# Optimization experiments

Measured on AMD Instinct MI355X. Metric: run time of the kernel, lower is better.

## Reference

```python
import jax, jax.numpy as jnp
import numpy as np

EPS = 1e-5  # BatchNorm2d default eps


def setup_inputs() -> dict:
    key = jax.random.key(0)
    k1, k2, k3, k4 = jax.random.split(key, 4)
    B, C, S, E = 2, 512, 256, 512  # C == E is required by the module's math
    x = jax.random.normal(k1, (B, C, S, E), dtype=jnp.float32)
    Q = jax.random.normal(k2, (E, E), dtype=jnp.float32)
    K = jax.random.normal(k3, (E, E), dtype=jnp.float32)
    V = jax.random.normal(k4, (E, E), dtype=jnp.float32)
    return {"x": x, "Q": Q, "K": K, "V": V}


def reference(x, Q, K, V):
    # BatchNorm2d(affine=False), training-mode batch stats over (B, H, W)
    mean = jnp.mean(x, axis=(0, 2, 3), keepdims=True)
    var = jnp.var(x, axis=(0, 2, 3), keepdims=True)  # biased, matches torch normalization
    xn = (x - mean) * jax.lax.rsqrt(var + EPS)

    divisor = jnp.sqrt(jnp.asarray(x.shape[-1], dtype=x.dtype))
    q = jnp.einsum('bcse,ef->bcsf', xn, Q)
    k = jnp.einsum('bcse,ef->bcsf', xn, K)
    v = jnp.einsum('bcse,ef->bcsf', xn, V)

    # scores: [B, C, S, S]
    prod = jnp.einsum('bcsf,bctf->bcst', q, k) / divisor
    # nn.Softmax2d softmaxes over the CHANNEL dim (axis 1)
    sm = jax.nn.softmax(prod, axis=1)
    attention = jnp.einsum('bcst,bctf->bcsf', sm, v)
    # dropout is identity in eval/reference mode; residual since E_in == E_out
    return attention + xn
```

## Files before the change

### kernel.cpp

```cpp
#include <hip/hip_runtime.h>
#include <hip/hip_bf16.h>
#include <cstdio>

#define Bn 2
#define Cn 512
#define Sn 256
#define En 512

typedef __attribute__((ext_vector_type(8))) short bf16x8;
typedef __attribute__((ext_vector_type(4))) float f32x4;

static constexpr size_t PROD_B = (1ull << 20);
static constexpr size_t V_B    = PROD_B + (256ull << 20);
static constexpr size_t ATH_B  = V_B + (256ull << 20);
static constexpr size_t ATL_B  = ATH_B + (512ull << 10);
static constexpr size_t VT_B   = ATL_B + (512ull << 10);
static constexpr size_t XNH_B  = VT_B + (512ull << 10);
static constexpr size_t XNL_B  = XNH_B + (256ull << 20);
static constexpr size_t WS_BIG = XNL_B + (256ull << 20);
static constexpr size_t SMT_B  = XNL_B;

__device__ __forceinline__ unsigned short f2bf(float f) {
  union { __hip_bfloat16 h; unsigned short u; } cv;
  cv.h = __float2bfloat16(f);
  return cv.u;
}
__device__ __forceinline__ float bf2f(unsigned short u) {
  union { unsigned int i; float f; } cv;
  cv.i = ((unsigned int)u) << 16;
  return cv.f;
}
__device__ __forceinline__ void split2(float v, unsigned short& h, unsigned short& l) {
  h = f2bf(v);
  l = f2bf(v - bf2f(h));
}
__device__ __forceinline__ int swzc(int row, int col) {
  return row * 64 + ((col & 3) | ((col & 60) ^ ((row & 7) << 3)));
}
__device__ __forceinline__ bf16x8 ldfrag(const unsigned short* arr, int row, int ks, int lane) {
  const int byte = (ks * 64 + ((lane >> 4) << 4)) ^ ((row & 7) << 4);
  return *(const bf16x8*)((const char*)(arr + (size_t)row * 64) + byte);
}
__device__ __forceinline__ f32x4 MFMA(bf16x8 a, bf16x8 b, f32x4 c) {
  return __builtin_amdgcn_mfma_f32_16x16x32_bf16(a, b, c, 0, 0, 0);
}
__device__ __forceinline__ void glds16(const void* g, void* l) {
  __builtin_amdgcn_global_load_lds(
      (const __attribute__((address_space(1))) unsigned int*)g,
      (__attribute__((address_space(3))) unsigned int*)l, 16, 0, 0);
}
__device__ __forceinline__ void stage_tile(const unsigned short* g, unsigned short* l,
                                           int nbytes, int wid, int lane, int nwaves) {
  const char* gb = (const char*)g;
  char* lb = (char*)l;
  for (int j = wid; j < (nbytes >> 10); j += nwaves)
    glds16(gb + j * 1024 + lane * 16, lb + j * 1024);
}

__global__ void k1_stats(const float* __restrict__ x, float* __restrict__ ws) {
  const int c = blockIdx.x, tid = threadIdx.x;
  const float4* p0 = (const float4*)(x + (size_t)c * (Sn * En));
  const float4* p1 = (const float4*)(x + (size_t)(Cn + c) * (Sn * En));
  float s1 = 0.f, s2 = 0.f;
  for (int i = tid; i < (Sn * En / 4); i += 256) {
    float4 a = p0[i], b = p1[i];
    s1 += (a.x + a.y) + (a.z + a.w) + (b.x + b.y) + (b.z + b.w);
    s2 += (a.x * a.x + a.y * a.y) + (a.z * a.z + a.w * a.w) +
          (b.x * b.x + b.y * b.y) + (b.z * b.z + b.w * b.w);
  }
  __shared__ float r1[256], r2[256];
  r1[tid] = s1; r2[tid] = s2;
  __syncthreads();
  for (int off = 128; off > 0; off >>= 1) {
    if (tid < off) { r1[tid] += r1[tid + off]; r2[tid] += r2[tid + off]; }
    __syncthreads();
  }
  if (tid == 0) {
    const float n = (float)(2 * Sn * En);
    float mean = r1[0] / n;
    float var = r2[0] / n - mean * mean;
    ws[c] = mean;
    ws[512 + c] = 1.0f / sqrtf(var + 1e-5f);
  }
}

__global__ void kA(const float* __restrict__ Q, const float* __restrict__ K,
                   const float* __restrict__ V, unsigned short* __restrict__ ATh,
                   unsigned short* __restrict__ ATl, unsigned short* __restrict__ VT) {
  const int f = blockIdx.x, tid = threadIdx.x;
  __shared__ float Kf[512];
  for (int i = tid; i < 512; i += 256) Kf[i] = K[(size_t)f * 512 + i];
  __syncthreads();
  const int fr64 = f & 63;
  const size_t atbase = ((size_t)(f >> 6) * 8) * 4096 + (size_t)fr64 * 64;
  const size_t vtbase = ((size_t)(f >> 7) * 8) * 8192 + (size_t)(f & 127) * 64;
#pragma unroll
  for (int half = 0; half < 2; ++half) {
    const int e = tid + half * 256;
    const float* Qe = Q + (size_t)e * 512;
    float acc = 0.f;
    for (int t = 0; t < 512; t += 4) {
      float4 q = *(const float4*)(Qe + t);
      acc += q.x * Kf[t] + q.y * Kf[t + 1] + q.z * Kf[t + 2] + q.w * Kf[t + 3];
    }
    unsigned short h, l;
    split2(acc, h, l);
    const int et = e >> 6, ec = e & 63;
    const int swa = (ec & 3) | ((ec & 60) ^ ((fr64 & 7) << 3));
    ATh[atbase + (size_t)et * 4096 + swa] = h;
    ATl[atbase + (size_t)et * 4096 + swa] = l;
    const int swv = (ec & 3) | ((ec & 60) ^ ((f & 7) << 3));
    VT[vtbase + (size_t)et * 8192 + swv] = f2bf(V[(size_t)e * 512 + f]);
  }
}

__global__ void kxn(const float* __restrict__ x, const float* __restrict__ ws,
                    unsigned short* __restrict__ XNh, unsigned short* __restrict__ XNl) {
  const int bid = blockIdx.x;
  const int bc = bid >> 1, half = bid & 1;
  const int c = bc & 511;
  const float mean = ws[c], rstd = ws[512 + c];
  const float* xb = x + (size_t)bc * 131072 + (size_t)half * 128 * 512;
  const int tid = threadIdx.x;
#pragma unroll 4
  for (int i = 0; i < 64; ++i) {
    const int g = tid + i * 256;
    const int r = g >> 7, c4 = g & 127;
    const float4 xv = *(const float4*)(xb + (size_t)r * 512 + c4 * 4);
    ushort4 hv, lv;
    split2((xv.x - mean) * rstd, hv.x, lv.x);
    split2((xv.y - mean) * rstd, hv.y, lv.y);
    split2((xv.z - mean) * rstd, hv.z, lv.z);
    split2((xv.w - mean) * rstd, hv.w, lv.w);
    const int et = c4 >> 4, colt4 = c4 & 15;
    const int row = half * 128 + r;
    const size_t idx = ((size_t)(bc * 8 + et) * 256 + row) * 64 +
                       ((colt4 * 4) ^ ((row & 7) << 3));
    *(ushort4*)&XNh[idx] = hv;
    *(ushort4*)&XNl[idx] = lv;
  }
}

__launch_bounds__(256)
__global__ void kv_proj(const unsigned short* __restrict__ VT,
                        const unsigned short* __restrict__ XNh_g,
                        unsigned short* __restrict__ vT_out) {
  __shared__ unsigned short BUF[2][16384];
  const int bid = blockIdx.x;
  const int L = (bid & 7) * 1024 + (bid >> 3);
  const int bc = L >> 3;
  const int fq = (L >> 1) & 3;
  const int th = L & 1;
  const int f0 = fq * 128, t0 = th * 128;
  const int tid = threadIdx.x, w = tid >> 6, lane = tid & 63;

  f32x4 acc[2][8];
#pragma unroll
  for (int i = 0; i < 2; ++i)
#pragma unroll
    for (int j = 0; j < 8; ++j) acc[i][j] = (f32x4){0.f, 0.f, 0.f, 0.f};

  stage_tile(VT + ((size_t)fq * 8 + 0) * 8192, &BUF[0][0], 16384, w, lane, 4);
  stage_tile(XNh_g + ((size_t)(bc * 8 + 0) * 256 + t0) * 64, &BUF[0][8192], 16384, w, lane, 4);
  __syncthreads();
#pragma unroll 1
  for (int et = 0; et < 8; ++et) {
    if (et < 7) {
      const int b = (et + 1) & 1;
      stage_tile(VT + ((size_t)fq * 8 + et + 1) * 8192, &BUF[b][0], 16384, w, lane, 4);
      stage_tile(XNh_g + ((size_t)(bc * 8 + et + 1) * 256 + t0) * 64, &BUF[b][8192],
                 16384, w, lane, 4);
    }
    const unsigned short* cb = &BUF[et & 1][0];
#pragma unroll
    for (int ks = 0; ks < 2; ++ks) {
      bf16x8 a0 = ldfrag(cb, w * 32 + (lane & 15), ks, lane);
      bf16x8 a1 = ldfrag(cb, w * 32 + 16 + (lane & 15), ks, lane);
#pragma unroll
      for (int ct = 0; ct < 8; ++ct) {
        bf16x8 b = ldfrag(cb + 8192, ct * 16 + (lane & 15), ks, lane);
        acc[0][ct] = MFMA(a0, b, acc[0][ct]);
        acc[1][ct] = MFMA(a1, b, acc[1][ct]);
      }
    }
    __syncthreads();
  }
#pragma unroll
  for (int rt = 0; rt < 2; ++rt)
#pragma unroll
    for (int ct = 0; ct < 8; ++ct)
#pragma unroll
      for (int r = 0; r < 4; ++r) {
        const int f = f0 + w * 32 + rt * 16 + (lane >> 4) * 4 + r;
        const int t = t0 + ct * 16 + (lane & 15);
        const size_t idx = (((size_t)bc * 4 + (f >> 7)) * 4 + (t >> 6)) * 8192 +
                           (size_t)(f & 127) * 64 +
                           ((t & 3) | ((t & 60) ^ ((f & 7) << 3)));
        vT_out[idx] = f2bf(acc[rt][ct][r]);
      }
}

__launch_bounds__(512, 2)
__global__ void kscores(const unsigned short* __restrict__ ATh_g,
                        const unsigned short* __restrict__ ATl_g,
                        const unsigned short* __restrict__ XNh_g,
                        const unsigned short* __restrict__ XNl_g,
                        float* __restrict__ prod) {
  __shared__ unsigned short STG[2][8192];
  __shared__ unsigned short YS[8][2048];
  const int bid = blockIdx.x;
  const int L = (bid & 7) * 256 + (bid >> 3);
  const int bc = L >> 1, half = L & 1;
  float* prodc = prod + (size_t)bc * 65536 + (size_t)half * 128 * 256;
  const int tid = threadIdx.x, w = tid >> 6, lane = tid & 63;
  const int lr = lane & 15, lk = lane >> 4;

  const int arow = half * 128 + w * 16 + lr;
  const unsigned short* xnh_row = XNh_g + ((size_t)bc * 8 * 256 + arow) * 64;
  const unsigned short* xnl_row = XNl_g + ((size_t)bc * 8 * 256 + arow) * 64;
  const int ac0 = (lk * 8) ^ ((arow & 7) << 3);
  const int ac1 = (32 + lk * 8) ^ ((arow & 7) << 3);

  f32x4 accz[16];
#pragma unroll
  for (int i = 0; i < 16; ++i) accz[i] = (f32x4){0.f, 0.f, 0.f, 0.f};
  f32x4 accy[4];
  unsigned short* const ys = YS[w];

  auto stAT = [&](int ftx, int et, int p) {
    stage_tile(ATh_g + ((size_t)ftx * 8 + et) * 4096, STG[p], 8192, w, lane, 8);
    stage_tile(ATl_g + ((size_t)ftx * 8 + et) * 4096, STG[p] + 4096, 8192, w, lane, 8);
  };
  auto stXT = [&](int ftx, int tq, int p) {
    stage_tile(XNh_g + ((size_t)(bc * 8 + ftx) * 256 + tq * 64) * 64, STG[p], 8192, w, lane, 8);
    stage_tile(XNl_g + ((size_t)(bc * 8 + ftx) * 256 + tq * 64) * 64, STG[p] + 4096, 8192, w, lane, 8);
  };
  auto ph1 = [&](int et, int p) {
#pragma unroll
    for (int ks = 0; ks < 2; ++ks) {
      const int ac = (ks ? ac1 : ac0);
      const bf16x8 ah = *(const bf16x8*)(xnh_row + (size_t)et * 16384 + ac);
      const bf16x8 al = *(const bf16x8*)(xnl_row + (size_t)et * 16384 + ac);
#pragma unroll
      for (int fc = 0; fc < 4; ++fc) {
        bf16x8 bh = ldfrag(STG[p], fc * 16 + lr, ks, lane);
        bf16x8 bl = ldfrag(STG[p] + 4096, fc * 16 + lr, ks, lane);
        accy[fc] = MFMA(ah, bh, accy[fc]);
        accy[fc] = MFMA(ah, bl, accy[fc]);
        accy[fc] = MFMA(al, bh, accy[fc]);
      }
    }
  };
  auto ph2 = [&](int z0, int p) {
#pragma unroll
    for (int ks = 0; ks < 2; ++ks) {
      bf16x8 yh = ldfrag(ys, lr, ks, lane);
      bf16x8 yl = ldfrag(ys + 1024, lr, ks, lane);
#pragma unroll
      for (int j = 0; j < 4; ++j) {
        bf16x8 bh = ldfrag(STG[p], j * 16 + lr, ks, lane);
        bf16x8 bl = ldfrag(STG[p] + 4096, j * 16 + lr, ks, lane);
        accz[z0 + j] = MFMA(yh, bh, accz[z0 + j]);
        accz[z0 + j] = MFMA(yh, bl, accz[z0 + j]);
        accz[z0 + j] = MFMA(yl, bh, accz[z0 + j]);
      }
    }
  };
  auto ywrite = [&]() {
#pragma unroll
    for (int fc = 0; fc < 4; ++fc)
#pragma unroll
      for (int r = 0; r < 4; ++r) {
        const int row = lk * 4 + r;
        const int col = fc * 16 + lr;
        unsigned short h, l;
        split2(accy[fc][r], h, l);
        const int idx = swzc(row, col);
        ys[idx] = h;
        ys[1024 + idx] = l;
      }
  };

  stAT(0, 0, 0);
  __syncthreads();

#pragma unroll 1
  for (int ft = 0; ft < 8; ++ft) {
#pragma unroll
    for (int i = 0; i < 4; ++i) accy[i] = (f32x4){0.f, 0.f, 0.f, 0.f};
    stAT(ft, 1, 1);                 ph1(0, 0); __syncthreads();
    stAT(ft, 2, 0);                 ph1(1, 1); __syncthreads();
    stAT(ft, 3, 1);                 ph1(2, 0); __syncthreads();
    stAT(ft, 4, 0);                 ph1(3, 1); __syncthreads();
    stAT(ft, 5, 1);                 ph1(4, 0); __syncthreads();
    stAT(ft, 6, 0);                 ph1(5, 1); __syncthreads();
    stAT(ft, 7, 1);                 ph1(6, 0); __syncthreads();
    stXT(ft, 0, 0);                 ph1(7, 1); __syncthreads();
    ywrite();
    stXT(ft, 1, 1);                 ph2(0, 0);  __syncthreads();
    stXT(ft, 2, 0);                 ph2(4, 1);  __syncthreads();
    stXT(ft, 3, 1);                 ph2(8, 0);  __syncthreads();
    if (ft < 7) stAT(ft + 1, 0, 0); ph2(12, 1); __syncthreads();
  }

  const float scale = 0.044194173824159216f;
#pragma unroll
  for (int i = 0; i < 16; ++i)
#pragma unroll
    for (int r = 0; r < 4; ++r) {
      const int row = w * 16 + lk * 4 + r;
      const int col = (i >> 2) * 64 + (i & 3) * 16 + lr;
      prodc[(size_t)row * 256 + col] = accz[i][r] * scale;
    }
}

__launch_bounds__(512)
__global__ void k3_softmax(const float* __restrict__ prodf, unsigned short* __restrict__ smT) {
  const int bid = blockIdx.x;
  const int b = bid >> 8, s = bid & 255;
  const int tid = threadIdx.x;
  const int t = tid & 255, ch = tid >> 8;
  const float* __restrict__ p =
      prodf + (size_t)b * (512ull * 65536) + (size_t)s * 256 + t + (size_t)ch * 256 * 65536;
  float m = -3.4e38f, sum = 0.f;
#pragma unroll 4
  for (int cc = 0; cc < 256; ++cc) {
    const float v = p[(size_t)cc * 65536];
    if (v > m) { sum *= __expf(m - v); m = v; }
    sum += __expf(v - m);
  }
  __shared__ float Ms[2][256], Ss[2][256];
  Ms[ch][t] = m; Ss[ch][t] = sum;
  __syncthreads();
  const float mo = Ms[ch ^ 1][t], so = Ss[ch ^ 1][t];
  const float mm = fmaxf(m, mo);
  const float inv = 1.0f / (sum * __expf(m - mm) + so * __expf(mo - mm));
  const int sh = s >> 7, r = s & 127, kt = t >> 6, col = t & 63;
  const int cidx = r * 64 + ((col & 3) | ((col & 60) ^ ((r & 7) << 3)));
  const size_t tbase = ((size_t)b * 512 + ch * 256) * 2 + sh;
#pragma unroll 4
  for (int cc = 0; cc < 256; ++cc) {
    const float ev = __expf(p[(size_t)cc * 65536] - mm) * inv;
    smT[((tbase + (size_t)cc * 2) * 4 + kt) * 8192 + cidx] = f2bf(ev);
  }
}

__launch_bounds__(256)
__global__ void k4_pv(const unsigned short* __restrict__ XNh_g,
                      const unsigned short* __restrict__ vT,
                      const unsigned short* __restrict__ smT,
                      float* __restrict__ out) {
  __shared__ unsigned short BUF[2][16384];
  const int bid = blockIdx.x;
  const int L = (bid & 7) * 1024 + (bid >> 3);
  const int bc = L >> 3;
  const int sh = (L >> 2) & 1;
  const int fh = L & 3;
  const int s0 = sh * 128, f0 = fh * 128;
  const int tid = threadIdx.x, w = tid >> 6, lane = tid & 63;

  f32x4 acc[2][8];
#pragma unroll
  for (int i = 0; i < 2; ++i)
#pragma unroll
    for (int j = 0; j < 8; ++j) acc[i][j] = (f32x4){0.f, 0.f, 0.f, 0.f};

  stage_tile(smT + (((size_t)bc * 2 + sh) * 4 + 0) * 8192, &BUF[0][0], 16384, w, lane, 4);
  stage_tile(vT + (((size_t)bc * 4 + fh) * 4 + 0) * 8192, &BUF[0][8192], 16384, w, lane, 4);
  __syncthreads();
#pragma unroll 1
  for (int kt = 0; kt < 4; ++kt) {
    if (kt < 3) {
      const int b = (kt + 1) & 1;
      stage_tile(smT + (((size_t)bc * 2 + sh) * 4 + kt + 1) * 8192, &BUF[b][0],
                 16384, w, lane, 4);
      stage_tile(vT + (((size_t)bc * 4 + fh) * 4 + kt + 1) * 8192, &BUF[b][8192],
                 16384, w, lane, 4);
    }
    const unsigned short* cb = &BUF[kt & 1][0];
#pragma unroll
    for (int ks = 0; ks < 2; ++ks) {
      bf16x8 a0 = ldfrag(cb, w * 32 + (lane & 15), ks, lane);
      bf16x8 a1 = ldfrag(cb, w * 32 + 16 + (lane & 15), ks, lane);
#pragma unroll
      for (int ct = 0; ct < 8; ++ct) {
        bf16x8 b = ldfrag(cb + 8192, ct * 16 + (lane & 15), ks, lane);
        acc[0][ct] = MFMA(a0, b, acc[0][ct]);
        acc[1][ct] = MFMA(a1, b, acc[1][ct]);
      }
    }
    __syncthreads();
  }
  const int lr = lane & 15, lk = lane >> 4;
#pragma unroll
  for (int rt = 0; rt < 2; ++rt)
#pragma unroll
    for (int ct = 0; ct < 8; ++ct)
#pragma unroll
      for (int r = 0; r < 4; ++r) {
        const int srow = s0 + w * 32 + rt * 16 + lk * 4 + r;
        const int fcol = f0 + ct * 16 + lr;
        const int et = fcol >> 6, col = fcol & 63;
        const unsigned short xh = XNh_g[((size_t)(bc * 8 + et) * 256 + srow) * 64 +
                                        ((col & 3) | ((col & 60) ^ ((srow & 7) << 3)))];
        const size_t oi = (size_t)bc * 131072 + (size_t)srow * 512 + fcol;
        out[oi] = acc[rt][ct][r] + bf2f(xh);
      }
}

extern "C" void kernel_launch(void* const* d_in, const int* in_sizes, int n_in,
                              void* d_out, int out_size, void* d_ws, size_t ws_size,
                              hipStream_t stream) {
  const float* x = (const float*)d_in[0];
  const float* Q = (const float*)d_in[1];
  const float* K = (const float*)d_in[2];
  const float* V = (const float*)d_in[3];
  float* out = (float*)d_out;
  float* ws = (float*)d_ws;
  float* prodf = (float*)((char*)d_ws + PROD_B);
  unsigned short* vT   = (unsigned short*)((char*)d_ws + V_B);
  unsigned short* ATh  = (unsigned short*)((char*)d_ws + ATH_B);
  unsigned short* ATl  = (unsigned short*)((char*)d_ws + ATL_B);
  unsigned short* VTm  = (unsigned short*)((char*)d_ws + VT_B);
  unsigned short* XNh  = (unsigned short*)((char*)d_ws + XNH_B);
  unsigned short* XNl  = (unsigned short*)((char*)d_ws + XNL_B);
  unsigned short* smT  = (unsigned short*)((char*)d_ws + SMT_B);
  if (ws_size < WS_BIG) {
    fprintf(stderr, "kernel_launch: ws_size %zu < needed %zu — expect corruption\n",
            ws_size, WS_BIG);
  }
  k1_stats<<<dim3(512), dim3(256), 0, stream>>>(x, ws);
  kA<<<dim3(512), dim3(256), 0, stream>>>(Q, K, V, ATh, ATl, VTm);
  kxn<<<dim3(2048), dim3(256), 0, stream>>>(x, ws, XNh, XNl);
  kv_proj<<<dim3(8192), dim3(256), 0, stream>>>(VTm, XNh, vT);
  kscores<<<dim3(2048), dim3(512), 0, stream>>>(ATh, ATl, XNh, XNl, prodf);
  k3_softmax<<<dim3(512), dim3(512), 0, stream>>>(prodf, smT);
  k4_pv<<<dim3(8192), dim3(256), 0, stream>>>(XNh, vT, smT, out);
}
```

Baseline: 1.887 ms.

## Restructure kscores to stage full AT and XN slabs with 32-wide F chunks

Reworks the scores kernel so each 64-wide feature chunk's A^T slice and the whole XN tile for that chunk are staged into large LDS buffers. The first GEMM then runs over all 8 E-tiles without a barrier between them, and the second GEMM consumes all 256 t columns per step. This cuts the number of __syncthreads and small staging rounds in the loop. In exchange LDS use rises to about 144 KB, the occupancy hint of 2 blocks per CU is dropped, and loads overlap less with compute because staging now happens at coarser points.

```diff
diff --git a/kernel.cpp b/kernel.cpp
--- a/kernel.cpp
+++ b/kernel.cpp
@@ -33,9 +33,6 @@
 __device__ __forceinline__ void split2(float v, unsigned short& h, unsigned short& l) {
   h = f2bf(v);
   l = f2bf(v - bf2f(h));
-}
-__device__ __forceinline__ int swzc(int row, int col) {
-  return row * 64 + ((col & 3) | ((col & 60) ^ ((row & 7) << 3)));
 }
 __device__ __forceinline__ bf16x8 ldfrag(const unsigned short* arr, int row, int ks, int lane) {
   const int byte = (ks * 64 + ((lane >> 4) << 4)) ^ ((row & 7) << 4);
@@ -200,14 +197,15 @@
       }
 }
 
-__launch_bounds__(512, 2)
+__launch_bounds__(512)
 __global__ void kscores(const unsigned short* __restrict__ ATh_g,
                         const unsigned short* __restrict__ ATl_g,
                         const unsigned short* __restrict__ XNh_g,
                         const unsigned short* __restrict__ XNl_g,
                         float* __restrict__ prod) {
-  __shared__ unsigned short STG[2][8192];
-  __shared__ unsigned short YS[8][2048];
+  __shared__ unsigned short ATS[32768];
+  __shared__ unsigned short XNS[32768];
+  __shared__ unsigned short YS[8][1024];
   const int bid = blockIdx.x;
   const int L = (bid & 7) * 256 + (bid >> 3);
   const int bc = L >> 1, half = L & 1;
@@ -218,99 +216,117 @@
   const int arow = half * 128 + w * 16 + lr;
   const unsigned short* xnh_row = XNh_g + ((size_t)bc * 8 * 256 + arow) * 64;
   const unsigned short* xnl_row = XNl_g + ((size_t)bc * 8 * 256 + arow) * 64;
-  const int ac0 = (lk * 8) ^ ((arow & 7) << 3);
+  const int ac0 = ((lk * 8)) ^ ((arow & 7) << 3);
   const int ac1 = (32 + lk * 8) ^ ((arow & 7) << 3);
 
   f32x4 accz[16];
 #pragma unroll
   for (int i = 0; i < 16; ++i) accz[i] = (f32x4){0.f, 0.f, 0.f, 0.f};
-  f32x4 accy[4];
-  unsigned short* const ys = YS[w];
-
-  auto stAT = [&](int ftx, int et, int p) {
-    stage_tile(ATh_g + ((size_t)ftx * 8 + et) * 4096, STG[p], 8192, w, lane, 8);
-    stage_tile(ATl_g + ((size_t)ftx * 8 + et) * 4096, STG[p] + 4096, 8192, w, lane, 8);
+  f32x4 accy[2];
+  unsigned short* const ys = &YS[w][0];
+
+  auto stATS = [&](int j) {
+    const int ft64 = j >> 1, hf = (j & 1) * 2048;
+    const char* gh = (const char*)(ATh_g + ((size_t)ft64 * 8 + w) * 4096 + hf);
+    const char* gl = (const char*)(ATl_g + ((size_t)ft64 * 8 + w) * 4096 + hf);
+    char* dh = (char*)(ATS + w * 2048);
+    char* dl = (char*)(ATS + 16384 + w * 2048);
+#pragma unroll
+    for (int r = 0; r < 4; ++r) {
+      glds16(gh + r * 1024 + lane * 16, dh + r * 1024);
+      glds16(gl + r * 1024 + lane * 16, dl + r * 1024);
+    }
   };
-  auto stXT = [&](int ftx, int tq, int p) {
-    stage_tile(XNh_g + ((size_t)(bc * 8 + ftx) * 256 + tq * 64) * 64, STG[p], 8192, w, lane, 8);
-    stage_tile(XNl_g + ((size_t)(bc * 8 + ftx) * 256 + tq * 64) * 64, STG[p] + 4096, 8192, w, lane, 8);
+  auto stXNS = [&](int fe) {
+    const char* gh = (const char*)(XNh_g + (size_t)(bc * 8 + fe) * 16384);
+    const char* gl = (const char*)(XNl_g + (size_t)(bc * 8 + fe) * 16384);
+#pragma unroll
+    for (int r = 0; r < 4; ++r) {
+      glds16(gh + (w * 4 + r) * 1024 + lane * 16, (char*)XNS + (w * 4 + r) * 1024);
+      glds16(gl + (w * 4 + r) * 1024 + lane * 16, (char*)(XNS + 16384) + (w * 4 + r) * 1024);
+    }
   };
-  auto ph1 = [&](int et, int p) {
-#pragma unroll
-    for (int ks = 0; ks < 2; ++ks) {
-      const int ac = (ks ? ac1 : ac0);
-      const bf16x8 ah = *(const bf16x8*)(xnh_row + (size_t)et * 16384 + ac);
-      const bf16x8 al = *(const bf16x8*)(xnl_row + (size_t)et * 16384 + ac);
-#pragma unroll
-      for (int fc = 0; fc < 4; ++fc) {
-        bf16x8 bh = ldfrag(STG[p], fc * 16 + lr, ks, lane);
-        bf16x8 bl = ldfrag(STG[p] + 4096, fc * 16 + lr, ks, lane);
-        accy[fc] = MFMA(ah, bh, accy[fc]);
-        accy[fc] = MFMA(ah, bl, accy[fc]);
-        accy[fc] = MFMA(al, bh, accy[fc]);
-      }
-    }
-  };
-  auto ph2 = [&](int z0, int p) {
-#pragma unroll
-    for (int ks = 0; ks < 2; ++ks) {
-      bf16x8 yh = ldfrag(ys, lr, ks, lane);
-      bf16x8 yl = ldfrag(ys + 1024, lr, ks, lane);
-#pragma unroll
-      for (int j = 0; j < 4; ++j) {
-        bf16x8 bh = ldfrag(STG[p], j * 16 + lr, ks, lane);
-        bf16x8 bl = ldfrag(STG[p] + 4096, j * 16 + lr, ks, lane);
-        accz[z0 + j] = MFMA(yh, bh, accz[z0 + j]);
-        accz[z0 + j] = MFMA(yh, bl, accz[z0 + j]);
-        accz[z0 + j] = MFMA(yl, bh, accz[z0 + j]);
+  auto ph1 = [&]() {
+#pragma unroll 2
+    for (int et = 0; et < 8; ++et) {
+      const unsigned short* ATSh = ATS + et * 2048;
+      const unsigned short* ATSl = ATS + 16384 + et * 2048;
+#pragma unroll
+      for (int ks = 0; ks < 2; ++ks) {
+        const int ac = (ks ? ac1 : ac0);
+        const bf16x8 ah = *(const bf16x8*)(xnh_row + (size_t)et * 16384 + ac);
+        const bf16x8 al = *(const bf16x8*)(xnl_row + (size_t)et * 16384 + ac);
+#pragma unroll
+        for (int fc = 0; fc < 2; ++fc) {
+          bf16x8 bh = ldfrag(ATSh, fc * 16 + lr, ks, lane);
+          bf16x8 bl = ldfrag(ATSl, fc * 16 + lr, ks, lane);
+          accy[fc] = MFMA(ah, bh, accy[fc]);
+          accy[fc] = MFMA(ah, bl, accy[fc]);
+          accy[fc] = MFMA(al, bh, accy[fc]);
+        }
       }
     }
   };
   auto ywrite = [&]() {
 #pragma unroll
-    for (int fc = 0; fc < 4; ++fc)
+    for (int fc = 0; fc < 2; ++fc)
 #pragma unroll
       for (int r = 0; r < 4; ++r) {
-        const int row = lk * 4 + r;
-        const int col = fc * 16 + lr;
         unsigned short h, l;
         split2(accy[fc][r], h, l);
-        const int idx = swzc(row, col);
+        const int idx = (lk * 4 + r) * 32 + fc * 16 + lr;
         ys[idx] = h;
-        ys[1024 + idx] = l;
+        ys[512 + idx] = l;
       }
   };
-
-  stAT(0, 0, 0);
+  auto ph2 = [&](int j) {
+    const int jo = (j & 1) * 64;
+    const bf16x8 yh = *(const bf16x8*)((const char*)ys + lr * 64 + lk * 16);
+    const bf16x8 yl = *(const bf16x8*)((const char*)ys + 1024 + lr * 64 + lk * 16);
+#pragma unroll
+    for (int ct = 0; ct < 16; ++ct) {
+      const int t = ct * 16 + lr;
+      const int byte = (jo + lk * 16) ^ ((t & 7) << 4);
+      const bf16x8 bh = *(const bf16x8*)((const char*)(XNS + (size_t)t * 64) + byte);
+      const bf16x8 bl = *(const bf16x8*)((const char*)(XNS + 16384 + (size_t)t * 64) + byte);
+      accz[ct] = MFMA(yh, bh, accz[ct]);
+      accz[ct] = MFMA(yh, bl, accz[ct]);
+      accz[ct] = MFMA(yl, bh, accz[ct]);
+    }
+  };
+
+  stXNS(0);
+  stATS(0);
   __syncthreads();
 
 #pragma unroll 1
-  for (int ft = 0; ft < 8; ++ft) {
-#pragma unroll
-    for (int i = 0; i < 4; ++i) accy[i] = (f32x4){0.f, 0.f, 0.f, 0.f};
-    stAT(ft, 1, 1);                 ph1(0, 0); __syncthreads();
-    stAT(ft, 2, 0);                 ph1(1, 1); __syncthreads();
-    stAT(ft, 3, 1);                 ph1(2, 0); __syncthreads();
-    stAT(ft, 4, 0);                 ph1(3, 1); __syncthreads();
-    stAT(ft, 5, 1);                 ph1(4, 0); __syncthreads();
-    stAT(ft, 6, 0);                 ph1(5, 1); __syncthreads();
-    stAT(ft, 7, 1);                 ph1(6, 0); __syncthreads();
-    stXT(ft, 0, 0);                 ph1(7, 1); __syncthreads();
+  for (int fe = 0; fe < 8; ++fe) {
+    accy[0] = (f32x4){0.f, 0.f, 0.f, 0.f};
+    accy[1] = (f32x4){0.f, 0.f, 0.f, 0.f};
+    ph1();
     ywrite();
-    stXT(ft, 1, 1);                 ph2(0, 0);  __syncthreads();
-    stXT(ft, 2, 0);                 ph2(4, 1);  __syncthreads();
-    stXT(ft, 3, 1);                 ph2(8, 0);  __syncthreads();
-    if (ft < 7) stAT(ft + 1, 0, 0); ph2(12, 1); __syncthreads();
+    __syncthreads();
+    stATS(2 * fe + 1);
+    ph2(2 * fe);
+    __syncthreads();
+    accy[0] = (f32x4){0.f, 0.f, 0.f, 0.f};
+    accy[1] = (f32x4){0.f, 0.f, 0.f, 0.f};
+    ph1();
+    ywrite();
+    __syncthreads();
+    if (fe < 7) stATS(2 * fe + 2);
+    ph2(2 * fe + 1);
+    __syncthreads();
+    if (fe < 7) stXNS(fe + 1);
   }
 
   const float scale = 0.044194173824159216f;
 #pragma unroll
-  for (int i = 0; i < 16; ++i)
+  for (int ct = 0; ct < 16; ++ct)
 #pragma unroll
     for (int r = 0; r < 4; ++r) {
       const int row = w * 16 + lk * 4 + r;
-      const int col = (i >> 2) * 64 + (i & 3) * 16 + lr;
-      prodc[(size_t)row * 256 + col] = accz[i][r] * scale;
+      prodc[(size_t)row * 256 + ct * 16 + lr] = accz[ct][r] * scale;
     }
 }
 
```

Result: slower. 2.317 ms (+22.8%).

## Double staging tile size in kscores to halve barrier count, add setprio

Applied to the files above, without the earlier changes.

The scores kernel now stages two E-tiles (or 128 T rows) per shared-memory buffer instead of one. This halves the number of __syncthreads barriers per ft iteration, from 12 to 6, and gives more MFMA work per barrier. The MFMA phases are also wrapped in s_setprio raises. The cost is twice the LDS for staging (64KB for STG plus 32KB for YS), which may limit occupancy at launch_bounds(512,2). The stage_tile stride argument changes to match the larger tiles.

```diff
diff --git a/kernel.cpp b/kernel.cpp
--- a/kernel.cpp
+++ b/kernel.cpp
@@ -206,7 +206,7 @@
                         const unsigned short* __restrict__ XNh_g,
                         const unsigned short* __restrict__ XNl_g,
                         float* __restrict__ prod) {
-  __shared__ unsigned short STG[2][8192];
+  __shared__ unsigned short STG[2][16384];
   __shared__ unsigned short YS[8][2048];
   const int bid = blockIdx.x;
   const int L = (bid & 7) * 256 + (bid >> 3);
@@ -225,46 +225,58 @@
 #pragma unroll
   for (int i = 0; i < 16; ++i) accz[i] = (f32x4){0.f, 0.f, 0.f, 0.f};
   f32x4 accy[4];
-  unsigned short* const ys = YS[w];
-
-  auto stAT = [&](int ftx, int et, int p) {
-    stage_tile(ATh_g + ((size_t)ftx * 8 + et) * 4096, STG[p], 8192, w, lane, 8);
-    stage_tile(ATl_g + ((size_t)ftx * 8 + et) * 4096, STG[p] + 4096, 8192, w, lane, 8);
+  unsigned short* const ys = &YS[w][0];
+
+  auto stAT2 = [&](int ftx, int et2, int p) {
+    stage_tile(ATh_g + ((size_t)ftx * 8 + et2) * 4096, STG[p], 16384, w, lane, 8);
+    stage_tile(ATl_g + ((size_t)ftx * 8 + et2) * 4096, STG[p] + 8192, 16384, w, lane, 8);
   };
-  auto stXT = [&](int ftx, int tq, int p) {
-    stage_tile(XNh_g + ((size_t)(bc * 8 + ftx) * 256 + tq * 64) * 64, STG[p], 8192, w, lane, 8);
-    stage_tile(XNl_g + ((size_t)(bc * 8 + ftx) * 256 + tq * 64) * 64, STG[p] + 4096, 8192, w, lane, 8);
+  auto stXT2 = [&](int ftx, int th, int p) {
+    stage_tile(XNh_g + ((size_t)(bc * 8 + ftx) * 256 + th * 128) * 64, STG[p],
+               16384, w, lane, 8);
+    stage_tile(XNl_g + ((size_t)(bc * 8 + ftx) * 256 + th * 128) * 64, STG[p] + 8192,
+               16384, w, lane, 8);
   };
-  auto ph1 = [&](int et, int p) {
-#pragma unroll
-    for (int ks = 0; ks < 2; ++ks) {
-      const int ac = (ks ? ac1 : ac0);
-      const bf16x8 ah = *(const bf16x8*)(xnh_row + (size_t)et * 16384 + ac);
-      const bf16x8 al = *(const bf16x8*)(xnl_row + (size_t)et * 16384 + ac);
-#pragma unroll
-      for (int fc = 0; fc < 4; ++fc) {
-        bf16x8 bh = ldfrag(STG[p], fc * 16 + lr, ks, lane);
-        bf16x8 bl = ldfrag(STG[p] + 4096, fc * 16 + lr, ks, lane);
-        accy[fc] = MFMA(ah, bh, accy[fc]);
-        accy[fc] = MFMA(ah, bl, accy[fc]);
-        accy[fc] = MFMA(al, bh, accy[fc]);
-      }
-    }
+  auto ph1pair = [&](int et2, int p) {
+    __builtin_amdgcn_s_setprio(1);
+#pragma unroll
+    for (int e2 = 0; e2 < 2; ++e2) {
+      const unsigned short* Bh = STG[p] + e2 * 4096;
+      const unsigned short* Bl = STG[p] + 8192 + e2 * 4096;
+      const size_t abase = (size_t)(et2 + e2) * 16384;
+#pragma unroll
+      for (int ks = 0; ks < 2; ++ks) {
+        const int ac = ks ? ac1 : ac0;
+        const bf16x8 ah = *(const bf16x8*)(xnh_row + abase + ac);
+        const bf16x8 al = *(const bf16x8*)(xnl_row + abase + ac);
+#pragma unroll
+        for (int fc = 0; fc < 4; ++fc) {
+          bf16x8 bh = ldfrag(Bh, fc * 16 + lr, ks, lane);
+          bf16x8 bl = ldfrag(Bl, fc * 16 + lr, ks, lane);
+          accy[fc] = MFMA(ah, bh, accy[fc]);
+          accy[fc] = MFMA(ah, bl, accy[fc]);
+          accy[fc] = MFMA(al, bh, accy[fc]);
+        }
+      }
+    }
+    __builtin_amdgcn_s_setprio(0);
   };
-  auto ph2 = [&](int z0, int p) {
+  auto ph2half = [&](int z0, int p) {
+    __builtin_amdgcn_s_setprio(1);
 #pragma unroll
     for (int ks = 0; ks < 2; ++ks) {
       bf16x8 yh = ldfrag(ys, lr, ks, lane);
       bf16x8 yl = ldfrag(ys + 1024, lr, ks, lane);
 #pragma unroll
-      for (int j = 0; j < 4; ++j) {
+      for (int j = 0; j < 8; ++j) {
         bf16x8 bh = ldfrag(STG[p], j * 16 + lr, ks, lane);
-        bf16x8 bl = ldfrag(STG[p] + 4096, j * 16 + lr, ks, lane);
+        bf16x8 bl = ldfrag(STG[p] + 8192, j * 16 + lr, ks, lane);
         accz[z0 + j] = MFMA(yh, bh, accz[z0 + j]);
         accz[z0 + j] = MFMA(yh, bl, accz[z0 + j]);
         accz[z0 + j] = MFMA(yl, bh, accz[z0 + j]);
       }
     }
+    __builtin_amdgcn_s_setprio(0);
   };
   auto ywrite = [&]() {
 #pragma unroll
@@ -281,37 +293,33 @@
       }
   };
 
-  stAT(0, 0, 0);
+  stAT2(0, 0, 0);
   __syncthreads();
 
 #pragma unroll 1
   for (int ft = 0; ft < 8; ++ft) {
 #pragma unroll
     for (int i = 0; i < 4; ++i) accy[i] = (f32x4){0.f, 0.f, 0.f, 0.f};
-    stAT(ft, 1, 1);                 ph1(0, 0); __syncthreads();
-    stAT(ft, 2, 0);                 ph1(1, 1); __syncthreads();
-    stAT(ft, 3, 1);                 ph1(2, 0); __syncthreads();
-    stAT(ft, 4, 0);                 ph1(3, 1); __syncthreads();
-    stAT(ft, 5, 1);                 ph1(4, 0); __syncthreads();
-    stAT(ft, 6, 0);                 ph1(5, 1); __syncthreads();
-    stAT(ft, 7, 1);                 ph1(6, 0); __syncthreads();
-    stXT(ft, 0, 0);                 ph1(7, 1); __syncthreads();
+    stAT2(ft, 2, 1);                 ph1pair(0, 0); __syncthreads();
+    stAT2(ft, 4, 0);                 ph1pair(2, 1); __syncthreads();
+    stAT2(ft, 6, 1);                 ph1pair(4, 0); __syncthreads();
+    stXT2(ft, 0, 0);                 ph1pair(6, 1); __syncthreads();
     ywrite();
-    stXT(ft, 1, 1);                 ph2(0, 0);  __syncthreads();
-    stXT(ft, 2, 0);                 ph2(4, 1);  __syncthreads();
-    stXT(ft, 3, 1);                 ph2(8, 0);  __syncthreads();
-    if (ft < 7) stAT(ft + 1, 0, 0); ph2(12, 1); __syncthreads();
+    stXT2(ft, 1, 1);                 ph2half(0, 0); __syncthreads();
+    if (ft < 7) stAT2(ft + 1, 0, 0); ph2half(8, 1); __syncthreads();
   }
 
   const float scale = 0.044194173824159216f;
 #pragma unroll
-  for (int i = 0; i < 16; ++i)
-#pragma unroll
-    for (int r = 0; r < 4; ++r) {
-      const int row = w * 16 + lk * 4 + r;
-      const int col = (i >> 2) * 64 + (i & 3) * 16 + lr;
-      prodc[(size_t)row * 256 + col] = accz[i][r] * scale;
-    }
+  for (int th = 0; th < 2; ++th)
+#pragma unroll
+    for (int ct = 0; ct < 8; ++ct)
+#pragma unroll
+      for (int r = 0; r < 4; ++r) {
+        const int row = w * 16 + lk * 4 + r;
+        prodc[(size_t)row * 256 + th * 128 + ct * 16 + lr] =
+            accz[th * 8 + ct][r] * scale;
+      }
 }
 
 __launch_bounds__(512)
```

Result: no change. 1.880 ms (-0.4%).
